# Kernel tuning notes

Measured on AMD Instinct MI355X. Metric: run time of the kernel, lower is better.

The kernel has to match this reference:

```python
import jax, jax.numpy as jnp
import numpy as np

B, T, D_IN, D_OUT = 4, 2048, 4096, 16384
MAX_INT = 127   # 2**(8-1) - 1
MIN_INT = -128  # -2**(8-1)
THRESH = 0.5
EPS = 1e-8


def setup_inputs() -> dict:
    key = jax.random.key(0)
    kx, kw, kb = jax.random.split(key, 3)
    x = jax.random.normal(kx, (B, T, D_IN), dtype=jnp.float32)
    # kaiming_uniform_(a=sqrt(5)) -> uniform(-1/sqrt(fan_in), 1/sqrt(fan_in))
    bound = 1.0 / np.sqrt(D_IN)
    weight = jax.random.uniform(kw, (D_OUT, D_IN), minval=-bound, maxval=bound, dtype=jnp.float32)
    bias = jax.random.uniform(kb, (D_OUT,), minval=-bound, maxval=bound, dtype=jnp.float32)
    return {"x": x, "weight": weight, "bias": bias}


def reference(x, weight, bias):
    # Per-token 8-bit absmax activation quantization (simulated)
    scale = jnp.max(jnp.abs(x), axis=-1, keepdims=True) / MAX_INT  # (B,T,1)
    x_int = jnp.clip(jnp.round(x / (scale + EPS)), MIN_INT, MAX_INT)
    x_q = x_int * scale
    # Ternary absmean weight quantization with STE
    w_scale = jnp.mean(jnp.abs(weight))
    w_scaled = weight / (w_scale + EPS)
    W_q = jnp.sign(w_scaled) * (jnp.abs(w_scaled) > THRESH).astype(weight.dtype)
    W_ste = weight + jax.lax.stop_gradient(W_q - weight)
    # Dense GEMM on dequantized values: (B,T,D_in) x (D_out,D_in)^T
    return jnp.einsum('btd,od->bto', x_q, W_ste) + bias
```

## Files before the change

kernel.cpp:

```cpp
#include <hip/hip_runtime.h>
#include <stdint.h>

#define B_DIM 4
#define T_DIM 2048
#define D_IN  4096
#define D_OUT 16384
#define M_DIM (B_DIM * T_DIM)
#define NW    ((size_t)D_OUT * (size_t)D_IN)

typedef __attribute__((ext_vector_type(4))) int v4i;

__global__ __launch_bounds__(256) void act_quant_kernel(
    const float* __restrict__ x, int8_t* __restrict__ xq,
    float* __restrict__ scales) {
  const int row = blockIdx.x;
  const float4* xr = (const float4*)(x + (size_t)row * D_IN);
  float4 v[4];
  float amax = 0.f;
#pragma unroll
  for (int c = 0; c < 4; ++c) {
    v[c] = xr[c * 256 + threadIdx.x];
    amax = fmaxf(amax, fmaxf(fmaxf(fabsf(v[c].x), fabsf(v[c].y)),
                             fmaxf(fabsf(v[c].z), fabsf(v[c].w))));
  }
#pragma unroll
  for (int off = 32; off > 0; off >>= 1)
    amax = fmaxf(amax, __shfl_down(amax, off, 64));
  __shared__ float smax[4];
  const int lane = threadIdx.x & 63, wave = threadIdx.x >> 6;
  if (lane == 0) smax[wave] = amax;
  __syncthreads();
  amax = fmaxf(fmaxf(smax[0], smax[1]), fmaxf(smax[2], smax[3]));
  const float scale = amax * (1.0f / 127.0f);
  const float denom = scale + 1e-8f;
  if (threadIdx.x == 0) scales[row] = scale;
  int* outp = (int*)(xq + (size_t)row * D_IN);
#pragma unroll
  for (int c = 0; c < 4; ++c) {
    int q0 = min(127, max(-128, __float2int_rn(v[c].x / denom)));
    int q1 = min(127, max(-128, __float2int_rn(v[c].y / denom)));
    int q2 = min(127, max(-128, __float2int_rn(v[c].z / denom)));
    int q3 = min(127, max(-128, __float2int_rn(v[c].w / denom)));
    outp[c * 256 + threadIdx.x] =
        (q0 & 255) | ((q1 & 255) << 8) | ((q2 & 255) << 16) | ((q3 & 255) << 24);
  }
}

__global__ __launch_bounds__(256) void wabs_kernel(const float* __restrict__ w,
                                                   double* __restrict__ out) {
  const float4* w4 = (const float4*)w;
  const size_t n4 = NW / 4;
  double acc = 0.0;
  for (size_t i = (size_t)blockIdx.x * blockDim.x + threadIdx.x; i < n4;
       i += (size_t)gridDim.x * blockDim.x) {
    float4 v = w4[i];
    acc += (double)fabsf(v.x) + (double)fabsf(v.y);
    acc += (double)fabsf(v.z) + (double)fabsf(v.w);
  }
#pragma unroll
  for (int off = 32; off > 0; off >>= 1) acc += __shfl_down(acc, off, 64);
  __shared__ double ssum[4];
  const int lane = threadIdx.x & 63, wave = threadIdx.x >> 6;
  if (lane == 0) ssum[wave] = acc;
  __syncthreads();
  if (threadIdx.x == 0) atomicAdd(out, ssum[0] + ssum[1] + ssum[2] + ssum[3]);
}

__global__ __launch_bounds__(256) void wquant_kernel(
    const float* __restrict__ w, const double* __restrict__ sumAbs,
    int8_t* __restrict__ wq) {
  const float ws = (float)(*sumAbs / (double)NW) + 1e-8f;
  const float4* w4 = (const float4*)w;
  int* outp = (int*)wq;
  const size_t stride = (size_t)gridDim.x * blockDim.x;
  size_t i = (size_t)blockIdx.x * blockDim.x + threadIdx.x;
#pragma unroll
  for (int c = 0; c < 4; ++c, i += stride) {
    float4 v = w4[i];
    float t0 = v.x / ws, t1 = v.y / ws, t2 = v.z / ws, t3 = v.w / ws;
    int q0 = (fabsf(t0) > 0.5f) ? ((t0 > 0.f) ? 1 : -1) : 0;
    int q1 = (fabsf(t1) > 0.5f) ? ((t1 > 0.f) ? 1 : -1) : 0;
    int q2 = (fabsf(t2) > 0.5f) ? ((t2 > 0.f) ? 1 : -1) : 0;
    int q3 = (fabsf(t3) > 0.5f) ? ((t3 > 0.f) ? 1 : -1) : 0;
    outp[i] = (q0 & 255) | ((q1 & 255) << 8) | ((q2 & 255) << 16) | ((q3 & 255) << 24);
  }
}

#define BM 128
#define BN 128
#define BK 64
#define KTILES (D_IN / BK)

__global__ __launch_bounds__(256) void gemm_i8_kernel(
    const int8_t* __restrict__ xq, const int8_t* __restrict__ wq,
    const float* __restrict__ scales, const float* __restrict__ bias,
    float* __restrict__ out) {
  __shared__ __align__(16) int8_t lA[BM * BK];
  __shared__ __align__(16) int8_t lB[BN * BK];

  const int tid = threadIdx.x;
  const int lane = tid & 63;
  const int wave = tid >> 6;
  const int wr = wave >> 1;
  const int wc = wave & 1;
  const int quad = lane >> 4;
  const int r16 = lane & 15;

  const int bm = blockIdx.y * BM;
  const int bn = blockIdx.x * BN;

  const int srow = tid >> 2;
  const int schunk = (tid & 3) ^ ((tid >> 3) & 3);
  const int8_t* gA = xq + (size_t)bm * D_IN;
  const int8_t* gB = wq + (size_t)bn * D_IN;

  const int fp = (quad ^ ((r16 >> 1) & 3)) * 16;

  v4i acc[4][4] = {};

  for (int kt = 0; kt < KTILES; ++kt) {
    const int k0 = kt * BK;
    __syncthreads();
#pragma unroll
    for (int i = 0; i < 2; ++i) {
      const int rl = i * 64 + srow;
      const size_t goff = (size_t)rl * D_IN + k0 + schunk * 16;
      __builtin_amdgcn_global_load_lds(
          (const __attribute__((address_space(1))) void*)(gA + goff),
          (__attribute__((address_space(3))) void*)(lA + i * 4096 + tid * 16),
          16, 0, 0);
      __builtin_amdgcn_global_load_lds(
          (const __attribute__((address_space(1))) void*)(gB + goff),
          (__attribute__((address_space(3))) void*)(lB + i * 4096 + tid * 16),
          16, 0, 0);
    }
    __syncthreads();

    v4i af[4], bf[4];
#pragma unroll
    for (int i = 0; i < 4; ++i) {
      const int m = wr * 64 + i * 16 + r16;
      af[i] = *(const v4i*)(lA + m * 64 + fp);
      const int n = wc * 64 + i * 16 + r16;
      bf[i] = *(const v4i*)(lB + n * 64 + fp);
    }
#pragma unroll
    for (int i = 0; i < 4; ++i)
#pragma unroll
      for (int j = 0; j < 4; ++j)
        acc[i][j] = __builtin_amdgcn_mfma_i32_16x16x64_i8(af[i], bf[j],
                                                          acc[i][j], 0, 0, 0);
  }

  float bs[4];
#pragma unroll
  for (int j = 0; j < 4; ++j) bs[j] = bias[bn + wc * 64 + j * 16 + r16];

#pragma unroll
  for (int i = 0; i < 4; ++i) {
#pragma unroll
    for (int reg = 0; reg < 4; ++reg) {
      const int m = bm + wr * 64 + i * 16 + quad * 4 + reg;
      const float s = scales[m];
      float* orow = out + (size_t)m * D_OUT + bn + wc * 64 + r16;
#pragma unroll
      for (int j = 0; j < 4; ++j) {
        orow[j * 16] = (float)acc[i][j][reg] * s + bs[j];
      }
    }
  }
}

extern "C" void kernel_launch(void* const* d_in, const int* in_sizes, int n_in,
                              void* d_out, int out_size, void* d_ws,
                              size_t ws_size, hipStream_t stream) {
  const float* x = (const float*)d_in[0];
  const float* w = (const float*)d_in[1];
  const float* bias = (const float*)d_in[2];
  float* out = (float*)d_out;

  char* ws = (char*)d_ws;
  double* d_sum = (double*)ws;
  float* d_scales = (float*)(ws + 256);
  int8_t* d_xq = (int8_t*)(ws + 33024);
  int8_t* d_wq = (int8_t*)(ws + 33024 + (size_t)M_DIM * D_IN);

  hipMemsetAsync(d_sum, 0, sizeof(double), stream);

  act_quant_kernel<<<M_DIM, 256, 0, stream>>>(x, d_xq, d_scales);
  wabs_kernel<<<2048, 256, 0, stream>>>(w, d_sum);
  wquant_kernel<<<16384, 256, 0, stream>>>(w, d_sum, d_wq);
  gemm_i8_kernel<<<dim3(D_OUT / BN, M_DIM / BM), 256, 0, stream>>>(
      d_xq, d_wq, d_scales, bias, out);
}
```

Before: 1.408 ms.

## Double GEMM K-tile to 128 and replace atomic weight-sum with two-stage reduction

The int8 GEMM now stages 128-wide K tiles in LDS with an 8-chunk XOR swizzle, running two MFMA sub-steps per tile. This halves the number of barrier pairs and load phases across the K loop. The weight absolute-sum drops its atomicAdd and memset: each block writes a partial sum, and a single-block kernel reduces the partials deterministically. The price is twice the LDS per block, which may lower occupancy, plus one extra kernel launch.

```diff
diff --git a/kernel.cpp b/kernel.cpp
--- a/kernel.cpp
+++ b/kernel.cpp
@@ -7,6 +7,7 @@
 #define D_OUT 16384
 #define M_DIM (B_DIM * T_DIM)
 #define NW    ((size_t)D_OUT * (size_t)D_IN)
+#define WABS_BLOCKS 2048
 
 typedef __attribute__((ext_vector_type(4))) int v4i;
 
@@ -47,7 +48,7 @@
 }
 
 __global__ __launch_bounds__(256) void wabs_kernel(const float* __restrict__ w,
-                                                   double* __restrict__ out) {
+                                                   double* __restrict__ partials) {
   const float4* w4 = (const float4*)w;
   const size_t n4 = NW / 4;
   double acc = 0.0;
@@ -63,7 +64,23 @@
   const int lane = threadIdx.x & 63, wave = threadIdx.x >> 6;
   if (lane == 0) ssum[wave] = acc;
   __syncthreads();
-  if (threadIdx.x == 0) atomicAdd(out, ssum[0] + ssum[1] + ssum[2] + ssum[3]);
+  if (threadIdx.x == 0)
+    partials[blockIdx.x] = ssum[0] + ssum[1] + ssum[2] + ssum[3];
+}
+
+__global__ __launch_bounds__(256) void wabs_reduce_kernel(
+    const double* __restrict__ partials, double* __restrict__ out) {
+  double acc = 0.0;
+#pragma unroll
+  for (int c = 0; c < WABS_BLOCKS / 256; ++c)
+    acc += partials[c * 256 + threadIdx.x];
+#pragma unroll
+  for (int off = 32; off > 0; off >>= 1) acc += __shfl_down(acc, off, 64);
+  __shared__ double ssum[4];
+  const int lane = threadIdx.x & 63, wave = threadIdx.x >> 6;
+  if (lane == 0) ssum[wave] = acc;
+  __syncthreads();
+  if (threadIdx.x == 0) *out = ssum[0] + ssum[1] + ssum[2] + ssum[3];
 }
 
 __global__ __launch_bounds__(256) void wquant_kernel(
@@ -88,7 +105,7 @@
 
 #define BM 128
 #define BN 128
-#define BK 64
+#define BK 128
 #define KTILES (D_IN / BK)
 
 __global__ __launch_bounds__(256) void gemm_i8_kernel(
@@ -109,12 +126,10 @@
   const int bm = blockIdx.y * BM;
   const int bn = blockIdx.x * BN;
 
-  const int srow = tid >> 2;
-  const int schunk = (tid & 3) ^ ((tid >> 3) & 3);
+  const int srow = tid >> 3;
+  const int schunk = (tid & 7) ^ ((tid >> 3) & 7);
   const int8_t* gA = xq + (size_t)bm * D_IN;
   const int8_t* gB = wq + (size_t)bn * D_IN;
-
-  const int fp = (quad ^ ((r16 >> 1) & 3)) * 16;
 
   v4i acc[4][4] = {};
 
@@ -122,8 +137,8 @@
     const int k0 = kt * BK;
     __syncthreads();
 #pragma unroll
-    for (int i = 0; i < 2; ++i) {
-      const int rl = i * 64 + srow;
+    for (int i = 0; i < 4; ++i) {
+      const int rl = i * 32 + srow;
       const size_t goff = (size_t)rl * D_IN + k0 + schunk * 16;
       __builtin_amdgcn_global_load_lds(
           (const __attribute__((address_space(1))) void*)(gA + goff),
@@ -136,20 +151,24 @@
     }
     __syncthreads();
 
-    v4i af[4], bf[4];
-#pragma unroll
-    for (int i = 0; i < 4; ++i) {
-      const int m = wr * 64 + i * 16 + r16;
-      af[i] = *(const v4i*)(lA + m * 64 + fp);
-      const int n = wc * 64 + i * 16 + r16;
-      bf[i] = *(const v4i*)(lB + n * 64 + fp);
+#pragma unroll
+    for (int s = 0; s < 2; ++s) {
+      v4i af[4], bf[4];
+#pragma unroll
+      for (int i = 0; i < 4; ++i) {
+        const int m = wr * 64 + i * 16 + r16;
+        const int pa = (((s << 2) | quad) ^ (r16 & 7)) * 16;
+        af[i] = *(const v4i*)(lA + m * BK + pa);
+        const int n = wc * 64 + i * 16 + r16;
+        bf[i] = *(const v4i*)(lB + n * BK + pa);
+      }
+#pragma unroll
+      for (int i = 0; i < 4; ++i)
+#pragma unroll
+        for (int j = 0; j < 4; ++j)
+          acc[i][j] = __builtin_amdgcn_mfma_i32_16x16x64_i8(af[i], bf[j],
+                                                            acc[i][j], 0, 0, 0);
     }
-#pragma unroll
-    for (int i = 0; i < 4; ++i)
-#pragma unroll
-      for (int j = 0; j < 4; ++j)
-        acc[i][j] = __builtin_amdgcn_mfma_i32_16x16x64_i8(af[i], bf[j],
-                                                          acc[i][j], 0, 0, 0);
   }
 
   float bs[4];
@@ -180,15 +199,15 @@
   float* out = (float*)d_out;
 
   char* ws = (char*)d_ws;
-  double* d_sum = (double*)ws;
-  float* d_scales = (float*)(ws + 256);
-  int8_t* d_xq = (int8_t*)(ws + 33024);
-  int8_t* d_wq = (int8_t*)(ws + 33024 + (size_t)M_DIM * D_IN);
-
-  hipMemsetAsync(d_sum, 0, sizeof(double), stream);
+  double* d_partials = (double*)ws;
+  double* d_sum = (double*)(ws + 16384);
+  float* d_scales = (float*)(ws + 16640);
+  int8_t* d_xq = (int8_t*)(ws + 49408);
+  int8_t* d_wq = (int8_t*)(ws + 49408 + (size_t)M_DIM * D_IN);
 
   act_quant_kernel<<<M_DIM, 256, 0, stream>>>(x, d_xq, d_scales);
-  wabs_kernel<<<2048, 256, 0, stream>>>(w, d_sum);
+  wabs_kernel<<<WABS_BLOCKS, 256, 0, stream>>>(w, d_partials);
+  wabs_reduce_kernel<<<1, 256, 0, stream>>>(d_partials, d_sum);
   wquant_kernel<<<16384, 256, 0, stream>>>(w, d_sum, d_wq);
   gemm_i8_kernel<<<dim3(D_OUT / BN, M_DIM / BM), 256, 0, stream>>>(
       d_xq, d_wq, d_scales, bias, out);
```

New measurement: 1.533 ms. 1.09x slower.
